# Kernel optimization log

Measured on AMD Instinct MI355X. Metric: run time of the kernel, lower is better.

## Reference

```python
import jax, jax.numpy as jnp
import numpy as np

N_ATOMS = 100000
K_NBR = 64
N_STRUCT = 32
HID = 128


def _energy(x, W1, w2, mask, batch_idx):
    # x: [N, K, 3] neighbor displacement vectors; surrogate per-edge energy MLP
    h = jnp.tanh(jnp.einsum('nkc,cd->nkd', x, W1))          # [N, K, HID]
    e = jnp.einsum('nkd,d->nk', h, w2)                       # [N, K]
    e = jnp.where(mask, 0.0, e)                              # zero padded neighbors
    per_atom = e.sum(axis=1)                                 # [N]
    return jax.ops.segment_sum(per_atom, batch_idx, num_segments=N_STRUCT)  # [S]


def setup_inputs() -> dict:
    key = jax.random.key(0)
    k = jax.random.split(key, 7)
    x = jax.random.normal(k[0], (N_ATOMS, K_NBR, 3), dtype=jnp.float32)
    neighbors_index = jax.random.randint(k[1], (K_NBR, N_ATOMS), 0, N_ATOMS)
    neighbors_pos = jax.random.randint(k[2], (N_ATOMS, K_NBR), 0, K_NBR)
    mask = jax.random.randint(k[3], (N_ATOMS, K_NBR), 0, 2).astype(bool)
    batch_idx = jax.random.randint(k[4], (N_ATOMS,), 0, N_STRUCT)
    W1 = jax.random.normal(k[5], (3, HID), dtype=jnp.float32) * 0.1
    w2 = jax.random.normal(k[6], (HID,), dtype=jnp.float32) * 0.1
    return {"x": x, "neighbors_index": neighbors_index, "neighbors_pos": neighbors_pos,
            "mask": mask, "batch_idx": batch_idx, "W1": W1, "w2": w2}


def reference(x, neighbors_index, neighbors_pos, mask, batch_idx, W1, w2):
    # predictions: per-structure scalar energies
    preds = _energy(x, W1, w2, mask, batch_idx)
    # grads = d(sum of predictions)/dx  (grad_outputs = ones_like(predictions))
    grads = jax.grad(lambda xx: _energy(xx, W1, w2, mask, batch_idx).sum())(x)  # [N, K, 3]
    nbr = neighbors_index.T                                   # [N, K]
    # irregular gather of reverse-edge gradients (uses UNMASKED grads, as in torch code)
    grads_messaged = grads[nbr, neighbors_pos]                # [N, K, 3]
    m = mask[..., None]
    first = jnp.where(m, 0.0, grads).sum(axis=1)              # [N, 3]
    second = jnp.where(m, 0.0, grads_messaged).sum(axis=1)    # [N, 3]
    forces = first - second
    return preds, forces
```

## Files before the change

kernel.cpp:

```cpp
#include <hip/hip_runtime.h>
#include <hip/hip_bf16.h>

#define N_ATOMS 100000
#define K_NBR   64
#define N_STRUCT 32
#define HID     128
#define N_EDGE  (N_ATOMS * K_NBR)
#define ATOMS_PB 32
#define EDGES_PB (ATOMS_PB * K_NBR)
#define NBLK_EL (N_ATOMS / ATOMS_PB)
#define NBLK_A  ((N_ATOMS + 63) / 64)

typedef unsigned int uint;
typedef unsigned long long ull;

#if __has_builtin(__builtin_amdgcn_exp2f)
#define EXP2(v) __builtin_amdgcn_exp2f(v)
#else
#define EXP2(v) __expf((v) * 0.69314718056f)
#endif

__device__ __forceinline__ uint bf_rne(float f) {
    uint u = __float_as_uint(f);
    return (u + 0x7fffu + ((u >> 16) & 1u)) >> 16;
}
__device__ __forceinline__ float ubf_lo(uint u) { return __uint_as_float(u << 16); }
__device__ __forceinline__ float ubf_hi(uint u) { return __uint_as_float(u & 0xffff0000u); }

__global__ void prep_kernel(const float* __restrict__ W1, const float* __restrict__ w2,
                            float4* __restrict__ pw4, float4* __restrict__ gw4,
                            float* __restrict__ sumw2)
{
    const float L2E2 = 2.885390082f;
    int d = threadIdx.x;
    float w0 = W1[d], w1 = W1[HID + d], wc = W1[2 * HID + d], wv = w2[d];
    pw4[d] = make_float4(L2E2 * w0, L2E2 * w1, L2E2 * wc, wv);
    gw4[d] = make_float4(4.f * wv * w0, 4.f * wv * w1, 4.f * wv * wc, 0.f);
    float v = wv;
    for (int off = 32; off; off >>= 1) v += __shfl_down(v, off, 64);
    __shared__ float sw_[2];
    if ((threadIdx.x & 63) == 0) sw_[threadIdx.x >> 6] = v;
    __syncthreads();
    if (threadIdx.x == 0) sumw2[0] = sw_[0] + sw_[1];
}

__global__ __launch_bounds__(256) void edge_local(
    const float* __restrict__ x, const int* __restrict__ mask,
    const int* __restrict__ batch,
    const float4* __restrict__ pw4, const float4* __restrict__ gw4,
    const float* __restrict__ sumw2p,
    uint2* __restrict__ gr8, ull* __restrict__ bm, float* __restrict__ part)
{
    __shared__ unsigned short list[EDGES_PB];
    __shared__ int   lcnt;
    __shared__ float sp[N_STRUCT];
    __shared__ int   sbatch[ATOMS_PB];

    const int tid = threadIdx.x, lane = tid & 63;
    const int ebase = blockIdx.x * EDGES_PB;

    if (tid == 0) lcnt = 0;
    if (tid < N_STRUCT) sp[tid] = 0.f;
    if (tid < ATOMS_PB) sbatch[tid] = batch[blockIdx.x * ATOMS_PB + tid];
    __syncthreads();

    #pragma unroll
    for (int p = 0; p < EDGES_PB / 256; ++p) {
        int le = p * 256 + tid;
        int m = mask[ebase + le];
        unsigned long long bal = __ballot(m == 0);
        int wcnt = __popcll(bal);
        int pre  = __popcll(bal & ((1ull << lane) - 1ull));
        int wbase;
        if (lane == 0) {
            wbase = atomicAdd(&lcnt, wcnt);
            bm[(ebase + le) >> 6] = bal;
        }
        wbase = __shfl(wbase, 0, 64);
        if (m == 0) list[wbase + pre] = (unsigned short)le;
        else        gr8[ebase + le] = make_uint2(0u, 0u);
    }
    __syncthreads();

    const int L = lcnt;
    const float sumw2 = sumw2p[0];

    for (int i = tid; i < L; i += 256) {
        int le  = list[i];
        int eid = ebase + le;
        const float* xp = x + (size_t)eid * 3;
        float x0 = xp[0], x1 = xp[1], x2 = xp[2];
        float rsum = 0.f, g0 = 0.f, g1 = 0.f, g2 = 0.f;
        for (int d = 0; d < HID; d += 4) {
            float4 wa = pw4[d], wb = pw4[d + 1], wc = pw4[d + 2], wd = pw4[d + 3];
            float4 Ga = gw4[d], Gb = gw4[d + 1], Gc = gw4[d + 2], Gd = gw4[d + 3];
            float ea = EXP2(fmaf(x0, wa.x, fmaf(x1, wa.y, x2 * wa.z)));
            float eb = EXP2(fmaf(x0, wb.x, fmaf(x1, wb.y, x2 * wb.z)));
            float ec = EXP2(fmaf(x0, wc.x, fmaf(x1, wc.y, x2 * wc.z)));
            float ed = EXP2(fmaf(x0, wd.x, fmaf(x1, wd.y, x2 * wd.z)));
            float aa = ea + 1.f, ab = eb + 1.f, ac = ec + 1.f, ad = ed + 1.f;
            float pab = aa * ab, pcd = ac * ad;
            float q   = __builtin_amdgcn_rcpf(pab * pcd);
            float qab = q * pcd, qcd = q * pab;
            float ra = qab * ab, rb = qab * aa, rc = qcd * ad, rd = qcd * ac;
            rsum = fmaf(wa.w, ra, rsum);
            rsum = fmaf(wb.w, rb, rsum);
            rsum = fmaf(wc.w, rc, rsum);
            rsum = fmaf(wd.w, rd, rsum);
            float sa = fmaf(-ra, ra, ra);
            float sb = fmaf(-rb, rb, rb);
            float sc = fmaf(-rc, rc, rc);
            float sd = fmaf(-rd, rd, rd);
            g0 = fmaf(sa, Ga.x, g0); g1 = fmaf(sa, Ga.y, g1); g2 = fmaf(sa, Ga.z, g2);
            g0 = fmaf(sb, Gb.x, g0); g1 = fmaf(sb, Gb.y, g1); g2 = fmaf(sb, Gb.z, g2);
            g0 = fmaf(sc, Gc.x, g0); g1 = fmaf(sc, Gc.y, g1); g2 = fmaf(sc, Gc.z, g2);
            g0 = fmaf(sd, Gd.x, g0); g1 = fmaf(sd, Gd.y, g1); g2 = fmaf(sd, Gd.z, g2);
        }
        float e = fmaf(-2.f, rsum, sumw2);
        uint lo = bf_rne(g0) | (bf_rne(g1) << 16);
        uint hi = bf_rne(g2);
        gr8[eid] = make_uint2(lo, hi);
        atomicAdd(&sp[sbatch[le >> 6]], e);
    }
    __syncthreads();
    if (tid < N_STRUCT) part[(size_t)tid * NBLK_EL + blockIdx.x] = sp[tid];
}

__global__ __launch_bounds__(256) void atom_fused(
    const uint2* __restrict__ gr8, const int* __restrict__ nidx,
    const int* __restrict__ pos,
    const ull* __restrict__ bm, const float* __restrict__ part,
    float* __restrict__ out)
{
    __shared__ int tile[64][65];
    __shared__ float sv[4];
    const int tid = threadIdx.x, lane = tid & 63, w = tid >> 6;
    const int n0 = blockIdx.x * 64;

    #pragma unroll
    for (int i = 0; i < 16; ++i) {
        int k = i * 4 + w, n = n0 + lane;
        tile[k][lane] = (n < N_ATOMS) ? nidx[k * N_ATOMS + n] : 0;
    }
    __syncthreads();

    #pragma unroll 2
    for (int j = 0; j < 8; ++j) {
        int nlA = w * 16 + 2 * j;
        int nA  = n0 + nlA;
        int nB  = nA + 1;
        bool vA = (nA < N_ATOMS), vB = (nB < N_ATOMS);

        float fA0 = 0.f, fA1 = 0.f, fA2 = 0.f, fB0 = 0.f, fB1 = 0.f, fB2 = 0.f;
        if (vA) {
            int eiA = nA * 64 + lane;
            ull mwA = bm[nA];
            uint2 aA = gr8[eiA];
            uint2 bA = make_uint2(0u, 0u);
            if ((mwA >> lane) & 1ull) {
                int gA = tile[lane][nlA] * 64 + pos[eiA];
                if ((bm[gA >> 6] >> (gA & 63)) & 1ull)
                    bA = gr8[gA];
            }
            fA0 = ubf_lo(aA.x) - ubf_lo(bA.x);
            fA1 = ubf_hi(aA.x) - ubf_hi(bA.x);
            fA2 = ubf_lo(aA.y) - ubf_lo(bA.y);
        }
        if (vB) {
            int eiB = nB * 64 + lane;
            ull mwB = bm[nB];
            uint2 aB = gr8[eiB];
            uint2 bB = make_uint2(0u, 0u);
            if ((mwB >> lane) & 1ull) {
                int gB = tile[lane][nlA + 1] * 64 + pos[eiB];
                if ((bm[gB >> 6] >> (gB & 63)) & 1ull)
                    bB = gr8[gB];
            }
            fB0 = ubf_lo(aB.x) - ubf_lo(bB.x);
            fB1 = ubf_hi(aB.x) - ubf_hi(bB.x);
            fB2 = ubf_lo(aB.y) - ubf_lo(bB.y);
        }

        for (int off = 32; off; off >>= 1) {
            fA0 += __shfl_down(fA0, off, 64);
            fA1 += __shfl_down(fA1, off, 64);
            fA2 += __shfl_down(fA2, off, 64);
            fB0 += __shfl_down(fB0, off, 64);
            fB1 += __shfl_down(fB1, off, 64);
            fB2 += __shfl_down(fB2, off, 64);
        }
        if (lane == 0 && vA) {
            float* fo = out + N_STRUCT + (size_t)nA * 3;
            fo[0] = fA0; fo[1] = fA1; fo[2] = fA2;
            if (vB) { fo[3] = fB0; fo[4] = fB1; fo[5] = fB2; }
        }
    }

    if (blockIdx.x < N_STRUCT) {
        int s = blockIdx.x;
        float v = 0.f;
        for (int i = tid; i < NBLK_EL; i += 256) v += part[(size_t)s * NBLK_EL + i];
        for (int off = 32; off; off >>= 1) v += __shfl_down(v, off, 64);
        if (lane == 0) sv[w] = v;
        __syncthreads();
        if (tid == 0) out[s] = sv[0] + sv[1] + sv[2] + sv[3];
    }
}

extern "C" void kernel_launch(void* const* d_in, const int* in_sizes, int n_in,
                              void* d_out, int out_size, void* d_ws, size_t ws_size,
                              hipStream_t stream)
{
    const float* x    = (const float*)d_in[0];
    const int*   nidx = (const int*)d_in[1];
    const int*   npos = (const int*)d_in[2];
    const int*   mask = (const int*)d_in[3];
    const int*   bidx = (const int*)d_in[4];
    const float* W1   = (const float*)d_in[5];
    const float* w2   = (const float*)d_in[6];
    float* out = (float*)d_out;

    char* ws = (char*)d_ws;
    uint2* gr8  = (uint2*)ws;
    ull*   bm   = (ull*)(ws + (size_t)N_EDGE * 8);
    float* part = (float*)(ws + (size_t)N_EDGE * 8 + (size_t)(N_EDGE / 64) * 8);
    char*  tail = ws + (size_t)N_EDGE * 8 + (size_t)(N_EDGE / 64) * 8
                     + (size_t)N_STRUCT * NBLK_EL * sizeof(float);
    float4* pw4   = (float4*)tail;
    float4* gw4   = (float4*)(tail + HID * 16);
    float*  sumw2 = (float*)(tail + 2 * HID * 16);

    hipLaunchKernelGGL(prep_kernel, dim3(1), dim3(128), 0, stream,
                       W1, w2, pw4, gw4, sumw2);
    hipLaunchKernelGGL(edge_local, dim3(NBLK_EL), dim3(256), 0, stream,
                       x, mask, bidx, pw4, gw4, sumw2, gr8, bm, part);
    hipLaunchKernelGGL(atom_fused, dim3(NBLK_A), dim3(256), 0, stream,
                       gr8, nidx, npos, bm, part, out);
}
```

Measured before the change: 369.3 us.

## Use packed fp16 dot2 for gradient accumulation and 16-lane atom reduction

The per-edge gradient accumulation in edge_local now packs the tanh-derivative terms into fp16 pairs and accumulates them with v_dot2 against precomputed fp16 weight pairs. This cuts the twelve FMAs per four hidden units down to six dot2 ops. The atom_fused kernel now handles four atoms per wavefront, with 16 lanes per atom each covering four neighbours, and reduces with DPP row shifts instead of a full 64-lane shuffle tree. This lowers reduction cost and packs more work into each wave, at the cost of reduced gradient precision from the fp16 inputs.

```diff
diff --git a/kernel.cpp b/kernel.cpp
--- a/kernel.cpp
+++ b/kernel.cpp
@@ -13,6 +13,8 @@
 
 typedef unsigned int uint;
 typedef unsigned long long ull;
+typedef _Float16 h2 __attribute__((ext_vector_type(2)));
+typedef __fp16  p2 __attribute__((ext_vector_type(2)));
 
 #if __has_builtin(__builtin_amdgcn_exp2f)
 #define EXP2(v) __builtin_amdgcn_exp2f(v)
@@ -20,6 +22,26 @@
 #define EXP2(v) __expf((v) * 0.69314718056f)
 #endif
 
+#if __has_builtin(__builtin_amdgcn_fdot2)
+#define FDOT2(a, b, c) __builtin_amdgcn_fdot2((a), (b), (c), false)
+#else
+__device__ __forceinline__ float FDOT2(h2 a, h2 b, float c) {
+    return fmaf((float)a.y, (float)b.y, fmaf((float)a.x, (float)b.x, c));
+}
+#endif
+
+union hcast { p2 p; h2 h; uint u; };
+
+__device__ __forceinline__ h2 pkh(float a, float b) {
+    hcast c; c.p = __builtin_amdgcn_cvt_pkrtz(a, b); return c.h;
+}
+__device__ __forceinline__ uint pku(float a, float b) {
+    hcast c; c.p = __builtin_amdgcn_cvt_pkrtz(a, b); return c.u;
+}
+__device__ __forceinline__ h2 u2h(uint u) {
+    hcast c; c.u = u; return c.h;
+}
+
 __device__ __forceinline__ uint bf_rne(float f) {
     uint u = __float_as_uint(f);
     return (u + 0x7fffu + ((u >> 16) & 1u)) >> 16;
@@ -27,27 +49,49 @@
 __device__ __forceinline__ float ubf_lo(uint u) { return __uint_as_float(u << 16); }
 __device__ __forceinline__ float ubf_hi(uint u) { return __uint_as_float(u & 0xffff0000u); }
 
+__device__ __forceinline__ float red16(float x) {
+    union { float f; int i; } a, b;
+    a.f = x;
+    b.i = __builtin_amdgcn_update_dpp(0, a.i, 0x118, 0xf, 0xf, false); a.f += b.f;
+    b.i = __builtin_amdgcn_update_dpp(0, a.i, 0x114, 0xf, 0xf, false); a.f += b.f;
+    b.i = __builtin_amdgcn_update_dpp(0, a.i, 0x112, 0xf, 0xf, false); a.f += b.f;
+    b.i = __builtin_amdgcn_update_dpp(0, a.i, 0x111, 0xf, 0xf, false); a.f += b.f;
+    return a.f;
+}
+
 __global__ void prep_kernel(const float* __restrict__ W1, const float* __restrict__ w2,
-                            float4* __restrict__ pw4, float4* __restrict__ gw4,
+                            float4* __restrict__ pw4, uint4* __restrict__ gh4,
                             float* __restrict__ sumw2)
 {
+    __shared__ float sgx[HID], sgy[HID], sgz[HID];
+    __shared__ float sw_[2];
     const float L2E2 = 2.885390082f;
     int d = threadIdx.x;
     float w0 = W1[d], w1 = W1[HID + d], wc = W1[2 * HID + d], wv = w2[d];
     pw4[d] = make_float4(L2E2 * w0, L2E2 * w1, L2E2 * wc, wv);
-    gw4[d] = make_float4(4.f * wv * w0, 4.f * wv * w1, 4.f * wv * wc, 0.f);
+    sgx[d] = 4.f * wv * w0; sgy[d] = 4.f * wv * w1; sgz[d] = 4.f * wv * wc;
     float v = wv;
     for (int off = 32; off; off >>= 1) v += __shfl_down(v, off, 64);
-    __shared__ float sw_[2];
-    if ((threadIdx.x & 63) == 0) sw_[threadIdx.x >> 6] = v;
-    __syncthreads();
-    if (threadIdx.x == 0) sumw2[0] = sw_[0] + sw_[1];
+    if ((d & 63) == 0) sw_[d >> 6] = v;
+    __syncthreads();
+    if (d == 0) sumw2[0] = sw_[0] + sw_[1];
+    if (d < HID / 4) {
+        int b = 4 * d;
+        uint c0 = pku(sgx[b],     sgx[b + 1]);
+        uint c1 = pku(sgx[b + 2], sgx[b + 3]);
+        uint c2 = pku(sgy[b],     sgy[b + 1]);
+        uint c3 = pku(sgy[b + 2], sgy[b + 3]);
+        uint c4 = pku(sgz[b],     sgz[b + 1]);
+        uint c5 = pku(sgz[b + 2], sgz[b + 3]);
+        gh4[2 * d]     = make_uint4(c0, c1, c2, c3);
+        gh4[2 * d + 1] = make_uint4(c4, c5, 0u, 0u);
+    }
 }
 
 __global__ __launch_bounds__(256) void edge_local(
     const float* __restrict__ x, const int* __restrict__ mask,
     const int* __restrict__ batch,
-    const float4* __restrict__ pw4, const float4* __restrict__ gw4,
+    const float4* __restrict__ pw4, const uint4* __restrict__ gh4,
     const float* __restrict__ sumw2p,
     uint2* __restrict__ gr8, ull* __restrict__ bm, float* __restrict__ part)
 {
@@ -93,7 +137,8 @@
         float rsum = 0.f, g0 = 0.f, g1 = 0.f, g2 = 0.f;
         for (int d = 0; d < HID; d += 4) {
             float4 wa = pw4[d], wb = pw4[d + 1], wc = pw4[d + 2], wd = pw4[d + 3];
-            float4 Ga = gw4[d], Gb = gw4[d + 1], Gc = gw4[d + 2], Gd = gw4[d + 3];
+            uint4 GA = gh4[(d >> 1)];
+            uint4 GB = gh4[(d >> 1) + 1];
             float ea = EXP2(fmaf(x0, wa.x, fmaf(x1, wa.y, x2 * wa.z)));
             float eb = EXP2(fmaf(x0, wb.x, fmaf(x1, wb.y, x2 * wb.z)));
             float ec = EXP2(fmaf(x0, wc.x, fmaf(x1, wc.y, x2 * wc.z)));
@@ -111,10 +156,14 @@
             float sb = fmaf(-rb, rb, rb);
             float sc = fmaf(-rc, rc, rc);
             float sd = fmaf(-rd, rd, rd);
-            g0 = fmaf(sa, Ga.x, g0); g1 = fmaf(sa, Ga.y, g1); g2 = fmaf(sa, Ga.z, g2);
-            g0 = fmaf(sb, Gb.x, g0); g1 = fmaf(sb, Gb.y, g1); g2 = fmaf(sb, Gb.z, g2);
-            g0 = fmaf(sc, Gc.x, g0); g1 = fmaf(sc, Gc.y, g1); g2 = fmaf(sc, Gc.z, g2);
-            g0 = fmaf(sd, Gd.x, g0); g1 = fmaf(sd, Gd.y, g1); g2 = fmaf(sd, Gd.z, g2);
+            h2 sab = pkh(sa, sb);
+            h2 scd = pkh(sc, sd);
+            g0 = FDOT2(sab, u2h(GA.x), g0);
+            g0 = FDOT2(scd, u2h(GA.y), g0);
+            g1 = FDOT2(sab, u2h(GA.z), g1);
+            g1 = FDOT2(scd, u2h(GA.w), g1);
+            g2 = FDOT2(sab, u2h(GB.x), g2);
+            g2 = FDOT2(scd, u2h(GB.y), g2);
         }
         float e = fmaf(-2.f, rsum, sumw2);
         uint lo = bf_rne(g0) | (bf_rne(g1) << 16);
@@ -144,55 +193,35 @@
     }
     __syncthreads();
 
+    const int grp = lane >> 4, kk = lane & 15;
+
     #pragma unroll 2
-    for (int j = 0; j < 8; ++j) {
-        int nlA = w * 16 + 2 * j;
-        int nA  = n0 + nlA;
-        int nB  = nA + 1;
-        bool vA = (nA < N_ATOMS), vB = (nB < N_ATOMS);
-
-        float fA0 = 0.f, fA1 = 0.f, fA2 = 0.f, fB0 = 0.f, fB1 = 0.f, fB2 = 0.f;
-        if (vA) {
-            int eiA = nA * 64 + lane;
-            ull mwA = bm[nA];
-            uint2 aA = gr8[eiA];
-            uint2 bA = make_uint2(0u, 0u);
-            if ((mwA >> lane) & 1ull) {
-                int gA = tile[lane][nlA] * 64 + pos[eiA];
-                if ((bm[gA >> 6] >> (gA & 63)) & 1ull)
-                    bA = gr8[gA];
+    for (int it = 0; it < 4; ++it) {
+        int nl = w * 16 + it * 4 + grp;
+        int n  = n0 + nl;
+        bool v = (n < N_ATOMS);
+        ull bmw = v ? bm[n] : 0ull;
+        float f0 = 0.f, f1 = 0.f, f2 = 0.f;
+        #pragma unroll
+        for (int ks = 0; ks < 4; ++ks) {
+            int k  = ks * 16 + kk;
+            int ei = n * 64 + k;
+            uint2 a = make_uint2(0u, 0u);
+            if (v) a = gr8[ei];
+            uint2 b = make_uint2(0u, 0u);
+            if ((bmw >> k) & 1ull) {
+                int g = tile[k][nl] * 64 + pos[ei];
+                if ((bm[g >> 6] >> (g & 63)) & 1ull)
+                    b = gr8[g];
             }
-            fA0 = ubf_lo(aA.x) - ubf_lo(bA.x);
-            fA1 = ubf_hi(aA.x) - ubf_hi(bA.x);
-            fA2 = ubf_lo(aA.y) - ubf_lo(bA.y);
-        }
-        if (vB) {
-            int eiB = nB * 64 + lane;
-            ull mwB = bm[nB];
-            uint2 aB = gr8[eiB];
-            uint2 bB = make_uint2(0u, 0u);
-            if ((mwB >> lane) & 1ull) {
-                int gB = tile[lane][nlA + 1] * 64 + pos[eiB];
-                if ((bm[gB >> 6] >> (gB & 63)) & 1ull)
-                    bB = gr8[gB];
-            }
-            fB0 = ubf_lo(aB.x) - ubf_lo(bB.x);
-            fB1 = ubf_hi(aB.x) - ubf_hi(bB.x);
-            fB2 = ubf_lo(aB.y) - ubf_lo(bB.y);
-        }
-
-        for (int off = 32; off; off >>= 1) {
-            fA0 += __shfl_down(fA0, off, 64);
-            fA1 += __shfl_down(fA1, off, 64);
-            fA2 += __shfl_down(fA2, off, 64);
-            fB0 += __shfl_down(fB0, off, 64);
-            fB1 += __shfl_down(fB1, off, 64);
-            fB2 += __shfl_down(fB2, off, 64);
-        }
-        if (lane == 0 && vA) {
-            float* fo = out + N_STRUCT + (size_t)nA * 3;
-            fo[0] = fA0; fo[1] = fA1; fo[2] = fA2;
-            if (vB) { fo[3] = fB0; fo[4] = fB1; fo[5] = fB2; }
+            f0 += ubf_lo(a.x) - ubf_lo(b.x);
+            f1 += ubf_hi(a.x) - ubf_hi(b.x);
+            f2 += ubf_lo(a.y) - ubf_lo(b.y);
+        }
+        f0 = red16(f0); f1 = red16(f1); f2 = red16(f2);
+        if (kk == 15 && v) {
+            float* fo = out + N_STRUCT + (size_t)n * 3;
+            fo[0] = f0; fo[1] = f1; fo[2] = f2;
         }
     }
 
@@ -227,13 +256,13 @@
     char*  tail = ws + (size_t)N_EDGE * 8 + (size_t)(N_EDGE / 64) * 8
                      + (size_t)N_STRUCT * NBLK_EL * sizeof(float);
     float4* pw4   = (float4*)tail;
-    float4* gw4   = (float4*)(tail + HID * 16);
+    uint4*  gh4   = (uint4*)(tail + HID * 16);
     float*  sumw2 = (float*)(tail + 2 * HID * 16);
 
     hipLaunchKernelGGL(prep_kernel, dim3(1), dim3(128), 0, stream,
-                       W1, w2, pw4, gw4, sumw2);
+                       W1, w2, pw4, gh4, sumw2);
     hipLaunchKernelGGL(edge_local, dim3(NBLK_EL), dim3(256), 0, stream,
-                       x, mask, bidx, pw4, gw4, sumw2, gr8, bm, part);
+                       x, mask, bidx, pw4, gh4, sumw2, gr8, bm, part);
     hipLaunchKernelGGL(atom_fused, dim3(NBLK_A), dim3(256), 0, stream,
                        gr8, nidx, npos, bm, part, out);
 }
```

New measurement: 345.6 us. 6.4% less time.
